# Kernel optimization log

Hardware: AMD Instinct MI355X
Metric: run time of the kernel (lower is better)

Reference implementation:

```python
import jax, jax.numpy as jnp
import numpy as np

C = 256
DK = C // 8  # query/key channels


def setup_inputs() -> dict:
    key = jax.random.key(0)
    ks = jax.random.split(key, 7)
    B, W, H = 4, 64, 64
    x = jax.random.normal(ks[0], (B, C, W, H), dtype=jnp.float32)
    s_in = 1.0 / np.sqrt(C)
    Wq = jax.random.normal(ks[1], (DK, C), dtype=jnp.float32) * s_in
    bq = jnp.zeros((DK,), dtype=jnp.float32)
    Wk = jax.random.normal(ks[2], (DK, C), dtype=jnp.float32) * s_in
    bk = jnp.zeros((DK,), dtype=jnp.float32)
    Wv = jax.random.normal(ks[3], (C, C), dtype=jnp.float32) * s_in
    bv = jnp.zeros((C,), dtype=jnp.float32)
    return {"x": x, "Wq": Wq, "bq": bq, "Wk": Wk, "bk": bk, "Wv": Wv, "bv": bv}


def reference(x, Wq, bq, Wk, bk, Wv, bv):
    B, Cc, W, H = x.shape
    N = W * H
    xf = x.reshape(B, Cc, N)  # (B, C, N) flattened spatial
    # 1x1 convs == channel matmuls
    q = jnp.einsum('dc,bcn->bnd', Wq, xf) + bq  # (B, N, DK)
    k = jnp.einsum('dc,bcn->bdn', Wk, xf) + bk[None, :, None]  # (B, DK, N)
    v = jnp.einsum('oc,bcn->bon', Wv, xf) + bv[None, :, None]  # (B, C, N)
    energy = jnp.einsum('bnd,bdm->bnm', q, k) / jnp.sqrt(jnp.float32(q.shape[-1]))
    attn = jax.nn.softmax(energy, axis=-1)  # (B, N, N)
    out = jnp.einsum('bcn,bmn->bcm', v, attn)  # v @ attn^T
    return out.reshape(B, Cc, W, H) + x
```

## Files before the change

kernel.cpp:

```cpp
#include <hip/hip_runtime.h>
#include <hip/hip_bf16.h>
#include <math.h>

#define BB 4
#define CC 256
#define DKK 32
#define NN 4096
#define QSCALE 0.17677669529663687f

typedef __attribute__((ext_vector_type(8))) __bf16 bf16x8;
typedef __attribute__((ext_vector_type(4))) __bf16 bf16x4;
typedef __attribute__((ext_vector_type(4))) float f32x4;

__global__ __launch_bounds__(256) void prep_kernel(
    const float* __restrict__ x, __bf16* __restrict__ xT,
    const float* __restrict__ Wq, const float* __restrict__ Wk,
    const float* __restrict__ Wv, __bf16* __restrict__ Wb)
{
    __shared__ float xs[64][68];
    const int tid = threadIdx.x;
    const int n0 = blockIdx.x * 64;
    const int c0 = blockIdx.y * 64;
    const int b  = blockIdx.z;

    if (b == 0) {
        int unit = blockIdx.y * 64 + blockIdx.x;
        if (unit < 80) {
            int i = (unit * 256 + tid) * 4;
            int row = i >> 8, col = i & 255;
            const float* src;
            if (row < 32)      src = &Wq[row * 256 + col];
            else if (row < 64) src = &Wk[(row - 32) * 256 + col];
            else               src = &Wv[(row - 64) * 256 + col];
            float4 v = *(const float4*)src;
            Wb[i]     = (__bf16)v.x;
            Wb[i + 1] = (__bf16)v.y;
            Wb[i + 2] = (__bf16)v.z;
            Wb[i + 3] = (__bf16)v.w;
        }
    }

#pragma unroll
    for (int p = 0; p < 4; p++) {
        int cc = p * 16 + (tid >> 4);
        int nf = (tid & 15) * 4;
        float4 v = *(const float4*)&x[((size_t)(b * CC + c0 + cc)) * NN + n0 + nf];
        xs[cc][nf] = v.x; xs[cc][nf + 1] = v.y; xs[cc][nf + 2] = v.z; xs[cc][nf + 3] = v.w;
    }
    __syncthreads();
    int n = tid >> 2, cs = (tid & 3) * 16;
    bf16x8 lo, hi;
#pragma unroll
    for (int j = 0; j < 8; j++) {
        lo[j] = (__bf16)xs[cs + j][n];
        hi[j] = (__bf16)xs[cs + 8 + j][n];
    }
    size_t base = ((size_t)(b * NN + n0 + n)) * CC + c0 + cs;
    *(bf16x8*)&xT[base]     = lo;
    *(bf16x8*)&xT[base + 8] = hi;
}

__global__ __launch_bounds__(256) void qkv_kernel(
    const __bf16* __restrict__ xT, const __bf16* __restrict__ Wb,
    const float* __restrict__ bq, const float* __restrict__ bk,
    const float* __restrict__ bv,
    __bf16* __restrict__ qws, __bf16* __restrict__ kws, __bf16* __restrict__ vws)
{
    __shared__ float scr[64][33];

    const int tid = threadIdx.x;
    const int w   = tid >> 6;
    const int l   = tid & 63;
    const int l15 = l & 15;
    const int lq  = l >> 4;
    const int n0  = blockIdx.x * 32;
    const int b   = blockIdx.y;

    const __bf16* xbase = xT + ((size_t)b * NN + n0 + l15) * CC + lq * 8;
    const __bf16* wbase = Wb + (size_t)(80 * w + l15) * CC + lq * 8;

    const f32x4 zf = {0.f, 0.f, 0.f, 0.f};
    f32x4 acc[5][2];
#pragma unroll
    for (int i = 0; i < 5; i++)
#pragma unroll
        for (int j = 0; j < 2; j++) acc[i][j] = zf;

    bf16x8 bcur[2], acur[5], bnxt[2], anxt[5];
#pragma unroll
    for (int nt = 0; nt < 2; nt++) bcur[nt] = *(const bf16x8*)(xbase + nt * 16 * CC);
#pragma unroll
    for (int ot = 0; ot < 5; ot++) acur[ot] = *(const bf16x8*)(wbase + ot * 16 * CC);

#pragma unroll
    for (int ks = 0; ks < 8; ks++) {
        if (ks < 7) {
#pragma unroll
            for (int nt = 0; nt < 2; nt++)
                bnxt[nt] = *(const bf16x8*)(xbase + nt * 16 * CC + (ks + 1) * 32);
#pragma unroll
            for (int ot = 0; ot < 5; ot++)
                anxt[ot] = *(const bf16x8*)(wbase + ot * 16 * CC + (ks + 1) * 32);
        }
#pragma unroll
        for (int ot = 0; ot < 5; ot++)
#pragma unroll
            for (int nt = 0; nt < 2; nt++)
                acc[ot][nt] = __builtin_amdgcn_mfma_f32_16x16x32_bf16(acur[ot], bcur[nt], acc[ot][nt], 0, 0, 0);
        if (ks < 7) {
#pragma unroll
            for (int nt = 0; nt < 2; nt++) bcur[nt] = bnxt[nt];
#pragma unroll
            for (int ot = 0; ot < 5; ot++) acur[ot] = anxt[ot];
        }
    }

    __bf16* vchunk = vws + (size_t)b * CC * NN + (size_t)(n0 >> 5) * 16 * 512;
#pragma unroll
    for (int ot = 0; ot < 5; ot++) {
        int ob = 80 * w + ot * 16;
#pragma unroll
        for (int nt = 0; nt < 2; nt++) {
#pragma unroll
            for (int r = 0; r < 4; r++) {
                int o = ob + lq * 4 + r;
                int n = nt * 16 + l15;
                float val = acc[ot][nt][r];
                if (ob >= 64) {
                    int c = o - 64;
                    vchunk[(5 * w - 4 + ot) * 512 + (lq * 4 + r) * 32 + n] =
                        (__bf16)(val + bv[c]);
                } else if (ob < 32) {
                    scr[o][n] = (val + bq[o]) * QSCALE;
                } else {
                    scr[o][n] = val + bk[o - 32];
                }
            }
        }
    }
    __syncthreads();
    {
        int n  = tid >> 3;
        int d0 = (tid & 7) * 4;
        bf16x4 qv, kv;
#pragma unroll
        for (int j = 0; j < 4; j++) {
            qv[j] = (__bf16)scr[d0 + j][n];
            kv[j] = (__bf16)scr[32 + d0 + j][n];
        }
        size_t base = ((size_t)b * NN + n0 + n) * DKK + d0;
        *(bf16x4*)&qws[base] = qv;
        *(bf16x4*)&kws[base] = kv;
    }
}

#define PST 40
#define MST 68
#define PWSZ (64 * PST)

__global__ __launch_bounds__(256, 2) void attn_kernel(
    const __bf16* __restrict__ qb, const __bf16* __restrict__ kb,
    const __bf16* __restrict__ vt, const float* __restrict__ x,
    float* __restrict__ out)
{
    __shared__ __align__(16) unsigned char smem[42240];
    __bf16* pw   = (__bf16*)smem + (threadIdx.x >> 6) * 2 * PWSZ;
    float*  Ls   = (float*)(smem + 40960);
    float*  Linv = (float*)(smem + 41984);

    const int tid = threadIdx.x;
    const int w   = tid >> 6;
    const int l   = tid & 63;
    const int l15 = l & 15;
    const int lq  = l >> 4;

    const int beta = blockIdx.x;
    const int b    = (beta >> 1) & 3;
    const int ch   = (beta >> 3) & 1;
    const int mt   = ((beta >> 4) << 1) | (beta & 1);
    const int m0   = mt * 64;

    const __bf16* qbb = qb + (size_t)b * NN * DKK;
    const __bf16* kbb = kb + (size_t)b * NN * DKK;
    const __bf16* vtb = vt + (size_t)b * CC * NN;

    bf16x8 qa[4];
#pragma unroll
    for (int af = 0; af < 4; af++)
        qa[af] = *(const bf16x8*)(qbb + (size_t)(m0 + af * 16 + l15) * DKK + lq * 8);

    const __bf16* kstrip = kbb + (size_t)(w * 32 + l15) * DKK + lq * 8;
    const __bf16* vstrip = vtb + (size_t)w * 8192 + (size_t)ch * 4096
                               + l15 * 32 + lq * 8;

    const f32x4 zf = {0.f, 0.f, 0.f, 0.f};
    f32x4 acc[4][8];
#pragma unroll
    for (int i = 0; i < 4; i++)
#pragma unroll
        for (int j = 0; j < 8; j++) acc[i][j] = zf;
    float lacc[4] = {0.f, 0.f, 0.f, 0.f};

    bf16x8 kA0 = *(const bf16x8*)kstrip;
    bf16x8 kA1 = *(const bf16x8*)(kstrip + 16 * DKK);
#pragma unroll
    for (int af = 0; af < 4; af++) {
        f32x4 e0 = __builtin_amdgcn_mfma_f32_16x16x32_bf16(kA0, qa[af], zf, 0, 0, 0);
        f32x4 e1 = __builtin_amdgcn_mfma_f32_16x16x32_bf16(kA1, qa[af], zf, 0, 0, 0);
        bf16x4 p0, p1;
#pragma unroll
        for (int r = 0; r < 4; r++) {
            float v0 = __expf(e0[r]); lacc[af] += v0; p0[r] = (__bf16)v0;
            float v1 = __expf(e1[r]); lacc[af] += v1; p1[r] = (__bf16)v1;
        }
        *(bf16x4*)&pw[(af * 16 + l15) * PST + lq * 4]      = p0;
        *(bf16x4*)&pw[(af * 16 + l15) * PST + 16 + lq * 4] = p1;
    }
    kA0 = *(const bf16x8*)(kstrip + (size_t)128 * DKK);
    kA1 = *(const bf16x8*)(kstrip + (size_t)144 * DKK);

#pragma unroll 2
    for (int ic = 0; ic < 31; ic++) {
        const int cur = ic & 1;
        const __bf16* vch = vstrip + (size_t)ic * 32768;

        bf16x8 vfC[4], vfN[4];
#pragma unroll
        for (int ct = 0; ct < 4; ct++)
            vfC[ct] = *(const bf16x8*)(vch + ct * 512);

        bf16x8 pf[4];
#pragma unroll
        for (int af = 0; af < 4; af++)
            pf[af] = *(const bf16x8*)&pw[cur * PWSZ + (af * 16 + l15) * PST + lq * 8];

#pragma unroll
        for (int af = 0; af < 4; af++) {
            f32x4 e0 = __builtin_amdgcn_mfma_f32_16x16x32_bf16(kA0, qa[af], zf, 0, 0, 0);
            f32x4 e1 = __builtin_amdgcn_mfma_f32_16x16x32_bf16(kA1, qa[af], zf, 0, 0, 0);
            bf16x4 p0, p1;
#pragma unroll
            for (int r = 0; r < 4; r++) {
                float v0 = __expf(e0[r]); lacc[af] += v0; p0[r] = (__bf16)v0;
                float v1 = __expf(e1[r]); lacc[af] += v1; p1[r] = (__bf16)v1;
            }
            *(bf16x4*)&pw[(cur ^ 1) * PWSZ + (af * 16 + l15) * PST + lq * 4]      = p0;
            *(bf16x4*)&pw[(cur ^ 1) * PWSZ + (af * 16 + l15) * PST + 16 + lq * 4] = p1;
        }
        kA0 = *(const bf16x8*)(kstrip + (size_t)(ic + 2) * 128 * DKK);
        kA1 = *(const bf16x8*)(kstrip + (size_t)((ic + 2) * 128 + 16) * DKK);

#pragma unroll
        for (int ct = 0; ct < 4; ct++)
            vfN[ct] = *(const bf16x8*)(vch + (4 + ct) * 512);
#pragma unroll
        for (int ct = 0; ct < 4; ct++)
#pragma unroll
            for (int af = 0; af < 4; af++)
                acc[af][ct] = __builtin_amdgcn_mfma_f32_16x16x32_bf16(vfC[ct], pf[af], acc[af][ct], 0, 0, 0);
#pragma unroll
        for (int ct = 0; ct < 4; ct++)
#pragma unroll
            for (int af = 0; af < 4; af++)
                acc[af][4 + ct] = __builtin_amdgcn_mfma_f32_16x16x32_bf16(vfN[ct], pf[af], acc[af][4 + ct], 0, 0, 0);
    }

    {
        const __bf16* vch = vstrip + (size_t)31 * 32768;
        bf16x8 pf[4];
#pragma unroll
        for (int af = 0; af < 4; af++)
            pf[af] = *(const bf16x8*)&pw[(31 & 1) * PWSZ + (af * 16 + l15) * PST + lq * 8];
        bf16x8 vfC[4], vfN[4];
#pragma unroll
        for (int ct = 0; ct < 4; ct++) vfC[ct] = *(const bf16x8*)(vch + ct * 512);
#pragma unroll
        for (int ct = 0; ct < 4; ct++) vfN[ct] = *(const bf16x8*)(vch + (4 + ct) * 512);
#pragma unroll
        for (int ct = 0; ct < 4; ct++)
#pragma unroll
            for (int af = 0; af < 4; af++)
                acc[af][ct] = __builtin_amdgcn_mfma_f32_16x16x32_bf16(vfC[ct], pf[af], acc[af][ct], 0, 0, 0);
#pragma unroll
        for (int ct = 0; ct < 4; ct++)
#pragma unroll
            for (int af = 0; af < 4; af++)
                acc[af][4 + ct] = __builtin_amdgcn_mfma_f32_16x16x32_bf16(vfN[ct], pf[af], acc[af][4 + ct], 0, 0, 0);
    }

#pragma unroll
    for (int af = 0; af < 4; af++) {
        lacc[af] += __shfl_xor(lacc[af], 16, 64);
        lacc[af] += __shfl_xor(lacc[af], 32, 64);
    }
    if (lq == 0) {
#pragma unroll
        for (int af = 0; af < 4; af++) Ls[w * 64 + af * 16 + l15] = lacc[af];
    }
    __syncthreads();
    if (tid < 64)
        Linv[tid] = 1.0f / (Ls[tid] + Ls[64 + tid] + Ls[128 + tid] + Ls[192 + tid]);

    float* Ored = (float*)smem + w * (32 * MST);
#pragma unroll
    for (int q = 0; q < 4; q++) {
        if (q > 0) __syncthreads();
#pragma unroll
        for (int ctp = 0; ctp < 2; ctp++) {
            int ct = 2 * q + ctp;
#pragma unroll
            for (int af = 0; af < 4; af++) {
#pragma unroll
                for (int r = 0; r < 4; r++)
                    Ored[(ctp * 16 + lq * 4 + r) * MST + af * 16 + l15] = acc[af][ct][r];
            }
        }
        __syncthreads();
        const int cl  = tid >> 3;
        const int mi0 = (tid & 7) * 8;
        const float* Ob = (const float*)smem + cl * MST;
#pragma unroll
        for (int j = 0; j < 2; j++) {
            int mi = mi0 + 4 * j;
            f32x4 s = *(const f32x4*)&Ob[mi];
            s = s + *(const f32x4*)&Ob[1 * (32 * MST) + mi];
            s = s + *(const f32x4*)&Ob[2 * (32 * MST) + mi];
            s = s + *(const f32x4*)&Ob[3 * (32 * MST) + mi];
            f32x4 li = *(const f32x4*)&Linv[mi];
            int c = ch * 128 + q * 32 + cl;
            size_t gi = ((size_t)(b * CC + c)) * NN + m0 + mi;
            f32x4 xr = *(const f32x4*)&x[gi];
            *(f32x4*)&out[gi] = s * li + xr;
        }
    }
}

extern "C" void kernel_launch(void* const* d_in, const int* in_sizes, int n_in,
                              void* d_out, int out_size, void* d_ws, size_t ws_size,
                              hipStream_t stream) {
    const float* x  = (const float*)d_in[0];
    const float* Wq = (const float*)d_in[1];
    const float* bq = (const float*)d_in[2];
    const float* Wk = (const float*)d_in[3];
    const float* bk = (const float*)d_in[4];
    const float* Wv = (const float*)d_in[5];
    const float* bv = (const float*)d_in[6];
    float* out = (float*)d_out;

    __bf16* qws = (__bf16*)d_ws;
    __bf16* kws = qws + (size_t)BB * NN * DKK;
    __bf16* vws = kws + (size_t)BB * NN * DKK;
    __bf16* Wb  = vws + (size_t)BB * CC * NN;
    __bf16* xT  = Wb  + (size_t)320 * CC;

    prep_kernel<<<dim3(64, 4, BB), 256, 0, stream>>>(x, xT, Wq, Wk, Wv, Wb);
    qkv_kernel <<<dim3(128, BB), 256, 0, stream>>>(xT, Wb, bq, bk, bv, qws, kws, vws);
    attn_kernel<<<dim3(512), 256, 0, stream>>>(qws, kws, vws, x, out);
}
```

Baseline: 151.8 us.

## Fuse transpose/bf16 prep into QKV projection kernel via shared-memory staging

Removes the separate prep kernel that transposed x and converted weights to bf16 in global memory. The QKV kernel now loads fp32 x directly, converts and transposes it into a padded shared tile, and converts fp32 weight rows to bf16 in registers on the fly. This saves one kernel launch and the round trip of the bf16 copy of x through global memory. In exchange, every block re-reads and re-converts the fp32 weights, and an extra barrier is needed because the shared buffer is reused for the output scratch.

Result: no change. 153.5 us (+1.2%).

```diff
diff --git a/kernel.cpp b/kernel.cpp
--- a/kernel.cpp
+++ b/kernel.cpp
@@ -12,61 +12,19 @@
 typedef __attribute__((ext_vector_type(4))) __bf16 bf16x4;
 typedef __attribute__((ext_vector_type(4))) float f32x4;
 
-__global__ __launch_bounds__(256) void prep_kernel(
-    const float* __restrict__ x, __bf16* __restrict__ xT,
+#define XROW 264
+
+__global__ __launch_bounds__(256) void qkv2_kernel(
+    const float* __restrict__ x,
     const float* __restrict__ Wq, const float* __restrict__ Wk,
-    const float* __restrict__ Wv, __bf16* __restrict__ Wb)
-{
-    __shared__ float xs[64][68];
-    const int tid = threadIdx.x;
-    const int n0 = blockIdx.x * 64;
-    const int c0 = blockIdx.y * 64;
-    const int b  = blockIdx.z;
-
-    if (b == 0) {
-        int unit = blockIdx.y * 64 + blockIdx.x;
-        if (unit < 80) {
-            int i = (unit * 256 + tid) * 4;
-            int row = i >> 8, col = i & 255;
-            const float* src;
-            if (row < 32)      src = &Wq[row * 256 + col];
-            else if (row < 64) src = &Wk[(row - 32) * 256 + col];
-            else               src = &Wv[(row - 64) * 256 + col];
-            float4 v = *(const float4*)src;
-            Wb[i]     = (__bf16)v.x;
-            Wb[i + 1] = (__bf16)v.y;
-            Wb[i + 2] = (__bf16)v.z;
-            Wb[i + 3] = (__bf16)v.w;
-        }
-    }
-
-#pragma unroll
-    for (int p = 0; p < 4; p++) {
-        int cc = p * 16 + (tid >> 4);
-        int nf = (tid & 15) * 4;
-        float4 v = *(const float4*)&x[((size_t)(b * CC + c0 + cc)) * NN + n0 + nf];
-        xs[cc][nf] = v.x; xs[cc][nf + 1] = v.y; xs[cc][nf + 2] = v.z; xs[cc][nf + 3] = v.w;
-    }
-    __syncthreads();
-    int n = tid >> 2, cs = (tid & 3) * 16;
-    bf16x8 lo, hi;
-#pragma unroll
-    for (int j = 0; j < 8; j++) {
-        lo[j] = (__bf16)xs[cs + j][n];
-        hi[j] = (__bf16)xs[cs + 8 + j][n];
-    }
-    size_t base = ((size_t)(b * NN + n0 + n)) * CC + c0 + cs;
-    *(bf16x8*)&xT[base]     = lo;
-    *(bf16x8*)&xT[base + 8] = hi;
-}
-
-__global__ __launch_bounds__(256) void qkv_kernel(
-    const __bf16* __restrict__ xT, const __bf16* __restrict__ Wb,
+    const float* __restrict__ Wv,
     const float* __restrict__ bq, const float* __restrict__ bk,
     const float* __restrict__ bv,
     __bf16* __restrict__ qws, __bf16* __restrict__ kws, __bf16* __restrict__ vws)
 {
-    __shared__ float scr[64][33];
+    __shared__ __align__(16) unsigned char smemB[32 * XROW * 2];
+    __bf16* xs = (__bf16*)smemB;
+    float (*scr)[33] = (float (*)[33])smemB;
 
     const int tid = threadIdx.x;
     const int w   = tid >> 6;
@@ -76,8 +34,32 @@
     const int n0  = blockIdx.x * 32;
     const int b   = blockIdx.y;
 
-    const __bf16* xbase = xT + ((size_t)b * NN + n0 + l15) * CC + lq * 8;
-    const __bf16* wbase = Wb + (size_t)(80 * w + l15) * CC + lq * 8;
+    {
+        const int cl = tid >> 3;
+        const int nf = (tid & 7) * 4;
+#pragma unroll
+        for (int p = 0; p < 8; p++) {
+            int c = p * 32 + cl;
+            float4 v = *(const float4*)&x[((size_t)(b * CC + c)) * NN + n0 + nf];
+            xs[(nf + 0) * XROW + c] = (__bf16)v.x;
+            xs[(nf + 1) * XROW + c] = (__bf16)v.y;
+            xs[(nf + 2) * XROW + c] = (__bf16)v.z;
+            xs[(nf + 3) * XROW + c] = (__bf16)v.w;
+        }
+    }
+
+    const float* wrow[5];
+#pragma unroll
+    for (int ot = 0; ot < 5; ot++) {
+        int ob = 80 * w + ot * 16;
+        const float* mat; int r0;
+        if (ob < 32)      { mat = Wq; r0 = ob; }
+        else if (ob < 64) { mat = Wk; r0 = ob - 32; }
+        else              { mat = Wv; r0 = ob - 64; }
+        wrow[ot] = mat + (size_t)(r0 + l15) * CC + lq * 8;
+    }
+
+    __syncthreads();
 
     const f32x4 zf = {0.f, 0.f, 0.f, 0.f};
     f32x4 acc[5][2];
@@ -86,21 +68,36 @@
 #pragma unroll
         for (int j = 0; j < 2; j++) acc[i][j] = zf;
 
+    const __bf16* xls = &xs[l15 * XROW + lq * 8];
+
     bf16x8 bcur[2], acur[5], bnxt[2], anxt[5];
 #pragma unroll
-    for (int nt = 0; nt < 2; nt++) bcur[nt] = *(const bf16x8*)(xbase + nt * 16 * CC);
-#pragma unroll
-    for (int ot = 0; ot < 5; ot++) acur[ot] = *(const bf16x8*)(wbase + ot * 16 * CC);
+    for (int nt = 0; nt < 2; nt++) bcur[nt] = *(const bf16x8*)(xls + nt * 16 * XROW);
+#pragma unroll
+    for (int ot = 0; ot < 5; ot++) {
+        f32x4 a0 = *(const f32x4*)(wrow[ot]);
+        f32x4 a1 = *(const f32x4*)(wrow[ot] + 4);
+        bf16x8 af;
+#pragma unroll
+        for (int j = 0; j < 4; j++) { af[j] = (__bf16)a0[j]; af[4 + j] = (__bf16)a1[j]; }
+        acur[ot] = af;
+    }
 
 #pragma unroll
     for (int ks = 0; ks < 8; ks++) {
         if (ks < 7) {
 #pragma unroll
             for (int nt = 0; nt < 2; nt++)
-                bnxt[nt] = *(const bf16x8*)(xbase + nt * 16 * CC + (ks + 1) * 32);
-#pragma unroll
-            for (int ot = 0; ot < 5; ot++)
-                anxt[ot] = *(const bf16x8*)(wbase + ot * 16 * CC + (ks + 1) * 32);
+                bnxt[nt] = *(const bf16x8*)(xls + nt * 16 * XROW + (ks + 1) * 32);
+#pragma unroll
+            for (int ot = 0; ot < 5; ot++) {
+                f32x4 a0 = *(const f32x4*)(wrow[ot] + (ks + 1) * 32);
+                f32x4 a1 = *(const f32x4*)(wrow[ot] + (ks + 1) * 32 + 4);
+                bf16x8 af;
+#pragma unroll
+                for (int j = 0; j < 4; j++) { af[j] = (__bf16)a0[j]; af[4 + j] = (__bf16)a1[j]; }
+                anxt[ot] = af;
+            }
         }
 #pragma unroll
         for (int ot = 0; ot < 5; ot++)
@@ -114,6 +111,8 @@
             for (int ot = 0; ot < 5; ot++) acur[ot] = anxt[ot];
         }
     }
+
+    __syncthreads();
 
     __bf16* vchunk = vws + (size_t)b * CC * NN + (size_t)(n0 >> 5) * 16 * 512;
 #pragma unroll
@@ -350,10 +349,8 @@
     __bf16* qws = (__bf16*)d_ws;
     __bf16* kws = qws + (size_t)BB * NN * DKK;
     __bf16* vws = kws + (size_t)BB * NN * DKK;
-    __bf16* Wb  = vws + (size_t)BB * CC * NN;
-    __bf16* xT  = Wb  + (size_t)320 * CC;
-
-    prep_kernel<<<dim3(64, 4, BB), 256, 0, stream>>>(x, xT, Wq, Wk, Wv, Wb);
-    qkv_kernel <<<dim3(128, BB), 256, 0, stream>>>(xT, Wb, bq, bk, bv, qws, kws, vws);
+
+    qkv2_kernel<<<dim3(128, BB), 256, 0, stream>>>(x, Wq, Wk, Wv, bq, bk, bv,
+                                                   qws, kws, vws);
     attn_kernel<<<dim3(512), 256, 0, stream>>>(qws, kws, vws, x, out);
 }
```
